# Kernel tuning notes

Hardware: AMD Instinct MI355X
Metric: run time of the kernel (lower is better)

The kernel has to match this reference:

```python
import jax, jax.numpy as jnp
import numpy as np


def setup_inputs() -> dict:
    key = jax.random.key(0)
    x = jax.random.normal(key, (4096, 512), dtype=jnp.float32)
    return {"x": x}


def reference(x):
    # Pairwise Euclidean distances for all (i, j) with i > j, flattened in the
    # same order as the original nested loop: (1,0),(2,0),(2,1),(3,0),...
    n = x.shape[0]
    sq = jnp.sum(x * x, axis=1)                      # [N]
    gram = x @ x.T                                   # [N, N]
    d2 = sq[:, None] + sq[None, :] - 2.0 * gram      # [N, N] squared dists
    ii, jj = jnp.tril_indices(n, k=-1)               # row-major lower triangle
    return jnp.sqrt(jnp.maximum(d2[ii, jj], 0.0))    # [N*(N-1)/2]
```

## Files before the change

kernel.cpp:

```cpp
#include <hip/hip_runtime.h>
#include <stdint.h>

#define N 4096
#define D 512
#define TILE 128
#define BK 128
#define KITERS (D / BK)
#define NB (N / TILE)
#define NOFF (NB * (NB - 1) / 2)
#define NBLK (NB * (NB + 1) / 2)

typedef float f32x4 __attribute__((ext_vector_type(4)));
typedef int   i32x8 __attribute__((ext_vector_type(8)));
typedef int   i32x4 __attribute__((ext_vector_type(4)));

__global__ __launch_bounds__(256) void prep_kernel(const float* __restrict__ x,
                                                   unsigned char* __restrict__ xq,
                                                   float* __restrict__ sq) {
    int row  = blockIdx.x * 4 + (threadIdx.x >> 6);
    int lane = threadIdx.x & 63;
    const float* xr = x + (size_t)row * D + lane * 8;
    float4 v0 = *reinterpret_cast<const float4*>(xr);
    float4 v1 = *reinterpret_cast<const float4*>(xr + 4);

    int w0 = __builtin_amdgcn_cvt_pk_fp8_f32(v0.x, v0.y, 0, false);
    w0     = __builtin_amdgcn_cvt_pk_fp8_f32(v0.z, v0.w, w0, true);
    int w1 = __builtin_amdgcn_cvt_pk_fp8_f32(v1.x, v1.y, 0, false);
    w1     = __builtin_amdgcn_cvt_pk_fp8_f32(v1.z, v1.w, w1, true);
    reinterpret_cast<int2*>(xq + (size_t)row * D)[lane] = make_int2(w0, w1);

    float s = v0.x * v0.x + v0.y * v0.y + v0.z * v0.z + v0.w * v0.w +
              v1.x * v1.x + v1.y * v1.y + v1.z * v1.z + v1.w * v1.w;
    #pragma unroll
    for (int off = 32; off > 0; off >>= 1) s += __shfl_down(s, off);
    if (lane == 0) sq[row] = s;
}

__global__ __launch_bounds__(512, 4) void pairdist_kernel(const unsigned char* __restrict__ xq,
                                                          const float* __restrict__ sq,
                                                          float* __restrict__ out) {
    __shared__ __align__(16) unsigned char As[TILE * BK];
    __shared__ __align__(16) unsigned char Bs[TILE * BK];

    int t = blockIdx.x;
    int bi, bj;
    if (t >= NOFF) {
        bi = bj = t - NOFF;
    } else {
        bi = (int)((sqrtf(8.0f * (float)t + 1.0f) + 1.0f) * 0.5f);
        while (bi * (bi - 1) / 2 > t) bi--;
        while ((bi + 1) * bi / 2 <= t) bi++;
        bj = t - bi * (bi - 1) / 2;
    }

    int tid  = threadIdx.x;
    int w    = tid >> 6;
    int lane = tid & 63;
    int quad = lane >> 4;
    int lr   = lane & 15;
    int wm   = w >> 1;
    int wn   = w & 1;

    const bool active = (bi != bj) || (wn == 0) || (wm >= 2);

    int srow   = lane >> 3;
    int schunk = lane & 7;
    int sw     = ((schunk ^ srow) << 4);
    const unsigned char* ga = xq + (size_t)(bi * TILE + w * 16 + srow) * D + sw;
    const unsigned char* gb = xq + (size_t)(bj * TILE + w * 16 + srow) * D + sw;
    unsigned char* la = As + w * 16 * BK;
    unsigned char* lb = Bs + w * 16 * BK;

    f32x4 acc[2][4];
    #pragma unroll
    for (int mt = 0; mt < 2; mt++)
        #pragma unroll
        for (int nt = 0; nt < 4; nt++)
            acc[mt][nt] = (f32x4)0.0f;

    for (int k0 = 0; k0 < D; k0 += BK) {
        __syncthreads();
        #pragma unroll
        for (int g = 0; g < 2; g++) {
            __builtin_amdgcn_global_load_lds(
                (const __attribute__((address_space(1))) void*)(ga + k0 + (size_t)g * 8 * D),
                (__attribute__((address_space(3))) void*)(la + g * 8 * BK), 16, 0, 0);
            __builtin_amdgcn_global_load_lds(
                (const __attribute__((address_space(1))) void*)(gb + k0 + (size_t)g * 8 * D),
                (__attribute__((address_space(3))) void*)(lb + g * 8 * BK), 16, 0, 0);
        }
        __syncthreads();

        if (active) {
            int c0 = (((2 * quad) ^ (lr & 7)) << 4);
            int c1 = c0 ^ 16;

            i32x8 af[2], bfr[4];
            #pragma unroll
            for (int mt = 0; mt < 2; mt++) {
                const unsigned char* rb = As + (wm * 32 + mt * 16 + lr) * BK;
                i32x4 lo = *reinterpret_cast<const i32x4*>(rb + c0);
                i32x4 hi = *reinterpret_cast<const i32x4*>(rb + c1);
                af[mt][0] = lo[0]; af[mt][1] = lo[1]; af[mt][2] = lo[2]; af[mt][3] = lo[3];
                af[mt][4] = hi[0]; af[mt][5] = hi[1]; af[mt][6] = hi[2]; af[mt][7] = hi[3];
            }
            #pragma unroll
            for (int nt = 0; nt < 4; nt++) {
                const unsigned char* rb = Bs + (wn * 64 + nt * 16 + lr) * BK;
                i32x4 lo = *reinterpret_cast<const i32x4*>(rb + c0);
                i32x4 hi = *reinterpret_cast<const i32x4*>(rb + c1);
                bfr[nt][0] = lo[0]; bfr[nt][1] = lo[1]; bfr[nt][2] = lo[2]; bfr[nt][3] = lo[3];
                bfr[nt][4] = hi[0]; bfr[nt][5] = hi[1]; bfr[nt][6] = hi[2]; bfr[nt][7] = hi[3];
            }

            #pragma unroll
            for (int mt = 0; mt < 2; mt++)
                #pragma unroll
                for (int nt = 0; nt < 4; nt++)
                    acc[mt][nt] = __builtin_amdgcn_mfma_scale_f32_16x16x128_f8f6f4(
                        af[mt], bfr[nt], acc[mt][nt],
                        0, 0,
                        0, 0x7F7F7F7F,
                        0, 0x7F7F7F7F);
        }
    }

    int ibase = bi * TILE + wm * 32;
    int jbase = bj * TILE + wn * 64;

    float sqi[2][4], sqj[4];
    #pragma unroll
    for (int mt = 0; mt < 2; mt++)
        #pragma unroll
        for (int tt = 0; tt < 4; tt++)
            sqi[mt][tt] = sq[ibase + mt * 16 + quad * 4 + tt];
    #pragma unroll
    for (int nt = 0; nt < 4; nt++)
        sqj[nt] = sq[jbase + nt * 16 + lr];

    if (bi != bj) {
        #pragma unroll
        for (int mt = 0; mt < 2; mt++) {
            #pragma unroll
            for (int tt = 0; tt < 4; tt++) {
                int i = ibase + mt * 16 + quad * 4 + tt;
                unsigned rowoff = (unsigned)(i * (i - 1) / 2);
                #pragma unroll
                for (int nt = 0; nt < 4; nt++) {
                    int j = jbase + nt * 16 + lr;
                    float d2 = sqi[mt][tt] + sqj[nt] - 2.0f * acc[mt][nt][tt];
                    out[rowoff + (unsigned)j] = __builtin_amdgcn_sqrtf(fmaxf(d2, 0.0f));
                }
            }
        }
    } else if (active) {
        #pragma unroll
        for (int mt = 0; mt < 2; mt++) {
            #pragma unroll
            for (int tt = 0; tt < 4; tt++) {
                int i = ibase + mt * 16 + quad * 4 + tt;
                unsigned rowoff = (unsigned)(i * (i - 1) / 2);
                #pragma unroll
                for (int nt = 0; nt < 4; nt++) {
                    int j = jbase + nt * 16 + lr;
                    if (j < i) {
                        float d2 = sqi[mt][tt] + sqj[nt] - 2.0f * acc[mt][nt][tt];
                        out[rowoff + (unsigned)j] = __builtin_amdgcn_sqrtf(fmaxf(d2, 0.0f));
                    }
                }
            }
        }
    }
}

extern "C" void kernel_launch(void* const* d_in, const int* in_sizes, int n_in,
                              void* d_out, int out_size, void* d_ws, size_t ws_size,
                              hipStream_t stream) {
    const float* x = (const float*)d_in[0];
    float* out = (float*)d_out;

    unsigned char* xq = (unsigned char*)d_ws;
    float* sq = (float*)((char*)d_ws + (size_t)N * D);

    prep_kernel<<<N / 4, 256, 0, stream>>>(x, xq, sq);

    pairdist_kernel<<<NBLK, 512, 0, stream>>>(xq, sq, out);
}
```

Baseline: 82.39 us.

## Switch to 64x128 rectangular tiles with 256-thread blocks for finer triangle coverage

Replaces the 128x128 square-tile triangular decomposition with 64-row by 128-column tiles processed by 4 waves per block, plus a new block-index-to-tile mapping that separates full tiles from diagonal partial tiles. The finer granularity wastes less work on the diagonal and yields more blocks for load balancing. In exchange each block reuses less data and issues more global-to-LDS traffic per output, and waves that are fully above the diagonal now exit early.

```diff
diff --git a/kernel.cpp b/kernel.cpp
--- a/kernel.cpp
+++ b/kernel.cpp
@@ -3,12 +3,14 @@
 
 #define N 4096
 #define D 512
-#define TILE 128
 #define BK 128
 #define KITERS (D / BK)
-#define NB (N / TILE)
-#define NOFF (NB * (NB - 1) / 2)
-#define NBLK (NB * (NB + 1) / 2)
+#define RG 64
+#define CP 128
+#define NRG (N / RG)
+#define NFULL 992
+#define NPART 64
+#define NBLK (NFULL + NPART)
 
 typedef float f32x4 __attribute__((ext_vector_type(4)));
 typedef int   i32x8 __attribute__((ext_vector_type(8)));
@@ -36,21 +38,24 @@
     if (lane == 0) sq[row] = s;
 }
 
-__global__ __launch_bounds__(512, 4) void pairdist_kernel(const unsigned char* __restrict__ xq,
+__global__ __launch_bounds__(256, 4) void pairdist_kernel(const unsigned char* __restrict__ xq,
                                                           const float* __restrict__ sq,
                                                           float* __restrict__ out) {
-    __shared__ __align__(16) unsigned char As[TILE * BK];
-    __shared__ __align__(16) unsigned char Bs[TILE * BK];
+    __shared__ __align__(16) unsigned char As[RG * BK];
+    __shared__ __align__(16) unsigned char Bs[CP * BK];
 
     int t = blockIdx.x;
-    int bi, bj;
-    if (t >= NOFF) {
-        bi = bj = t - NOFF;
+    int ri, cj;
+    if (t >= NFULL) {
+        int p = t - NFULL;
+        ri = p;
+        cj = p >> 1;
     } else {
-        bi = (int)((sqrtf(8.0f * (float)t + 1.0f) + 1.0f) * 0.5f);
-        while (bi * (bi - 1) / 2 > t) bi--;
-        while ((bi + 1) * bi / 2 <= t) bi++;
-        bj = t - bi * (bi - 1) / 2;
+        int a = (int)((sqrtf(4.0f * (float)t + 1.0f) + 1.0f) * 0.5f);
+        while (a * (a - 1) > t) a--;
+        while (a * (a + 1) <= t) a++;
+        if (t < a * a) { ri = 2 * a;     cj = t - a * (a - 1); }
+        else           { ri = 2 * a + 1; cj = t - a * a; }
     }
 
     int tid  = threadIdx.x;
@@ -61,15 +66,17 @@
     int wm   = w >> 1;
     int wn   = w & 1;
 
-    const bool active = (bi != bj) || (wn == 0) || (wm >= 2);
+    int ibase = ri * RG + wm * 32;
+    int jbase = cj * CP + wn * 64;
+    const bool active = (jbase <= ibase + 31);
 
     int srow   = lane >> 3;
     int schunk = lane & 7;
     int sw     = ((schunk ^ srow) << 4);
-    const unsigned char* ga = xq + (size_t)(bi * TILE + w * 16 + srow) * D + sw;
-    const unsigned char* gb = xq + (size_t)(bj * TILE + w * 16 + srow) * D + sw;
+    const unsigned char* ga = xq + (size_t)(ri * RG + w * 16 + srow) * D + sw;
+    const unsigned char* gb = xq + (size_t)(cj * CP + w * 32 + srow) * D + sw;
     unsigned char* la = As + w * 16 * BK;
-    unsigned char* lb = Bs + w * 16 * BK;
+    unsigned char* lb = Bs + w * 32 * BK;
 
     f32x4 acc[2][4];
     #pragma unroll
@@ -81,14 +88,15 @@
     for (int k0 = 0; k0 < D; k0 += BK) {
         __syncthreads();
         #pragma unroll
-        for (int g = 0; g < 2; g++) {
+        for (int g = 0; g < 2; g++)
             __builtin_amdgcn_global_load_lds(
                 (const __attribute__((address_space(1))) void*)(ga + k0 + (size_t)g * 8 * D),
                 (__attribute__((address_space(3))) void*)(la + g * 8 * BK), 16, 0, 0);
+        #pragma unroll
+        for (int g = 0; g < 4; g++)
             __builtin_amdgcn_global_load_lds(
                 (const __attribute__((address_space(1))) void*)(gb + k0 + (size_t)g * 8 * D),
                 (__attribute__((address_space(3))) void*)(lb + g * 8 * BK), 16, 0, 0);
-        }
         __syncthreads();
 
         if (active) {
@@ -125,8 +133,7 @@
         }
     }
 
-    int ibase = bi * TILE + wm * 32;
-    int jbase = bj * TILE + wn * 64;
+    if (!active) return;
 
     float sqi[2][4], sqj[4];
     #pragma unroll
@@ -138,7 +145,7 @@
     for (int nt = 0; nt < 4; nt++)
         sqj[nt] = sq[jbase + nt * 16 + lr];
 
-    if (bi != bj) {
+    if (jbase + 63 < ibase) {
         #pragma unroll
         for (int mt = 0; mt < 2; mt++) {
             #pragma unroll
@@ -153,7 +160,7 @@
                 }
             }
         }
-    } else if (active) {
+    } else {
         #pragma unroll
         for (int mt = 0; mt < 2; mt++) {
             #pragma unroll
@@ -184,5 +191,5 @@
 
     prep_kernel<<<N / 4, 256, 0, stream>>>(x, xq, sq);
 
-    pairdist_kernel<<<NBLK, 512, 0, stream>>>(xq, sq, out);
+    pairdist_kernel<<<NBLK, 256, 0, stream>>>(xq, sq, out);
 }
```

After: 81.28 us. About the same (-1.4%).

## Load MFMA fragments directly from global memory, dropping LDS staging and barriers

Applied to the files above, without the earlier changes.

Removes the shared-memory tiles and the per-iteration __syncthreads; each wave now reads its fp8 A/B fragments straight from global memory into registers, relying on L1/L2 for reuse across waves. Inactive waves on diagonal tiles return early, and fully-below-diagonal waves on diagonal tiles skip the per-element mask. This removes barrier and LDS traffic but raises redundant global/L2 reads, since tiles are no longer shared between the waves that use the same rows.

```diff
diff --git a/kernel.cpp b/kernel.cpp
--- a/kernel.cpp
+++ b/kernel.cpp
@@ -39,9 +39,6 @@
 __global__ __launch_bounds__(512, 4) void pairdist_kernel(const unsigned char* __restrict__ xq,
                                                           const float* __restrict__ sq,
                                                           float* __restrict__ out) {
-    __shared__ __align__(16) unsigned char As[TILE * BK];
-    __shared__ __align__(16) unsigned char Bs[TILE * BK];
-
     int t = blockIdx.x;
     int bi, bj;
     if (t >= NOFF) {
@@ -61,15 +58,11 @@
     int wm   = w >> 1;
     int wn   = w & 1;
 
+    int ibase = bi * TILE + wm * 32;
+    int jbase = bj * TILE + wn * 64;
+
     const bool active = (bi != bj) || (wn == 0) || (wm >= 2);
-
-    int srow   = lane >> 3;
-    int schunk = lane & 7;
-    int sw     = ((schunk ^ srow) << 4);
-    const unsigned char* ga = xq + (size_t)(bi * TILE + w * 16 + srow) * D + sw;
-    const unsigned char* gb = xq + (size_t)(bj * TILE + w * 16 + srow) * D + sw;
-    unsigned char* la = As + w * 16 * BK;
-    unsigned char* lb = Bs + w * 16 * BK;
+    const bool fullwave = (bi != bj) || (jbase + 63 < ibase);
 
     f32x4 acc[2][4];
     #pragma unroll
@@ -78,37 +71,27 @@
         for (int nt = 0; nt < 4; nt++)
             acc[mt][nt] = (f32x4)0.0f;
 
-    for (int k0 = 0; k0 < D; k0 += BK) {
-        __syncthreads();
+    if (active) {
+        const unsigned char* arow = xq + (size_t)(ibase + lr) * D + quad * 32;
+        const unsigned char* brow = xq + (size_t)(jbase + lr) * D + quad * 32;
+
         #pragma unroll
-        for (int g = 0; g < 2; g++) {
-            __builtin_amdgcn_global_load_lds(
-                (const __attribute__((address_space(1))) void*)(ga + k0 + (size_t)g * 8 * D),
-                (__attribute__((address_space(3))) void*)(la + g * 8 * BK), 16, 0, 0);
-            __builtin_amdgcn_global_load_lds(
-                (const __attribute__((address_space(1))) void*)(gb + k0 + (size_t)g * 8 * D),
-                (__attribute__((address_space(3))) void*)(lb + g * 8 * BK), 16, 0, 0);
-        }
-        __syncthreads();
-
-        if (active) {
-            int c0 = (((2 * quad) ^ (lr & 7)) << 4);
-            int c1 = c0 ^ 16;
-
+        for (int it = 0; it < KITERS; it++) {
+            const int k0 = it * BK;
             i32x8 af[2], bfr[4];
             #pragma unroll
             for (int mt = 0; mt < 2; mt++) {
-                const unsigned char* rb = As + (wm * 32 + mt * 16 + lr) * BK;
-                i32x4 lo = *reinterpret_cast<const i32x4*>(rb + c0);
-                i32x4 hi = *reinterpret_cast<const i32x4*>(rb + c1);
+                const unsigned char* p = arow + (size_t)(mt * 16) * D + k0;
+                i32x4 lo = *reinterpret_cast<const i32x4*>(p);
+                i32x4 hi = *reinterpret_cast<const i32x4*>(p + 16);
                 af[mt][0] = lo[0]; af[mt][1] = lo[1]; af[mt][2] = lo[2]; af[mt][3] = lo[3];
                 af[mt][4] = hi[0]; af[mt][5] = hi[1]; af[mt][6] = hi[2]; af[mt][7] = hi[3];
             }
             #pragma unroll
             for (int nt = 0; nt < 4; nt++) {
-                const unsigned char* rb = Bs + (wn * 64 + nt * 16 + lr) * BK;
-                i32x4 lo = *reinterpret_cast<const i32x4*>(rb + c0);
-                i32x4 hi = *reinterpret_cast<const i32x4*>(rb + c1);
+                const unsigned char* p = brow + (size_t)(nt * 16) * D + k0;
+                i32x4 lo = *reinterpret_cast<const i32x4*>(p);
+                i32x4 hi = *reinterpret_cast<const i32x4*>(p + 16);
                 bfr[nt][0] = lo[0]; bfr[nt][1] = lo[1]; bfr[nt][2] = lo[2]; bfr[nt][3] = lo[3];
                 bfr[nt][4] = hi[0]; bfr[nt][5] = hi[1]; bfr[nt][6] = hi[2]; bfr[nt][7] = hi[3];
             }
@@ -125,8 +108,7 @@
         }
     }
 
-    int ibase = bi * TILE + wm * 32;
-    int jbase = bj * TILE + wn * 64;
+    if (!active) return;
 
     float sqi[2][4], sqj[4];
     #pragma unroll
@@ -138,7 +120,7 @@
     for (int nt = 0; nt < 4; nt++)
         sqj[nt] = sq[jbase + nt * 16 + lr];
 
-    if (bi != bj) {
+    if (fullwave) {
         #pragma unroll
         for (int mt = 0; mt < 2; mt++) {
             #pragma unroll
@@ -153,7 +135,7 @@
                 }
             }
         }
-    } else if (active) {
+    } else {
         #pragma unroll
         for (int mt = 0; mt < 2; mt++) {
             #pragma unroll
```

Result: slower. 99.57 us (+20.8%).

## Give each wavefront an independent 32x64 triangular tile with private LDS

Applied to the files above, without the earlier changes.

Replaces the 128x128 block tiling, in which 8 waves share LDS tiles and synchronize with __syncthreads, with a per-wave decomposition. Each wavefront independently owns a 32x64 output tile, enumerated over the lower triangle so that diagonal blocks no longer carry idle waves. Each wave stages its own A/B slices through its own LDS region using global_load_lds and explicit waitcnt, and prefetches the next K slice while issuing MFMAs. This removes block-wide barriers and the wasted diagonal work, but loses operand sharing between waves, so global/L2 traffic increases and the hand-written waitcnt encodings carry correctness risk.

```diff
diff --git a/kernel.cpp b/kernel.cpp
--- a/kernel.cpp
+++ b/kernel.cpp
@@ -3,12 +3,13 @@
 
 #define N 4096
 #define D 512
-#define TILE 128
 #define BK 128
 #define KITERS (D / BK)
-#define NB (N / TILE)
-#define NOFF (NB * (NB - 1) / 2)
-#define NBLK (NB * (NB + 1) / 2)
+#define WTM 32
+#define WTN 64
+#define NGI (N / WTM)
+#define NTW 4160
+#define GRID (NTW / 4)
 
 typedef float f32x4 __attribute__((ext_vector_type(4)));
 typedef int   i32x8 __attribute__((ext_vector_type(8)));
@@ -36,40 +37,41 @@
     if (lane == 0) sq[row] = s;
 }
 
-__global__ __launch_bounds__(512, 4) void pairdist_kernel(const unsigned char* __restrict__ xq,
+__global__ __launch_bounds__(256, 3) void pairdist_kernel(const unsigned char* __restrict__ xq,
                                                           const float* __restrict__ sq,
                                                           float* __restrict__ out) {
-    __shared__ __align__(16) unsigned char As[TILE * BK];
-    __shared__ __align__(16) unsigned char Bs[TILE * BK];
-
-    int t = blockIdx.x;
-    int bi, bj;
-    if (t >= NOFF) {
-        bi = bj = t - NOFF;
-    } else {
-        bi = (int)((sqrtf(8.0f * (float)t + 1.0f) + 1.0f) * 0.5f);
-        while (bi * (bi - 1) / 2 > t) bi--;
-        while ((bi + 1) * bi / 2 <= t) bi++;
-        bj = t - bi * (bi - 1) / 2;
-    }
+    __shared__ __align__(16) unsigned char lds[4][12 * 1024];
 
     int tid  = threadIdx.x;
     int w    = tid >> 6;
     int lane = tid & 63;
     int quad = lane >> 4;
     int lr   = lane & 15;
-    int wm   = w >> 1;
-    int wn   = w & 1;
-
-    const bool active = (bi != bj) || (wn == 0) || (wm >= 2);
+
+    int t = blockIdx.x * 4 + w;
+
+    int a = (int)((sqrtf(4.0f * (float)t + 1.0f) - 1.0f) * 0.5f);
+    while (a * (a + 1) > t) a--;
+    while ((a + 1) * (a + 2) <= t) a++;
+    int gi, jg;
+    int r0 = t - a * (a + 1);
+    if (r0 <= a) { gi = 2 * a;     jg = r0; }
+    else         { gi = 2 * a + 1; jg = t - (a + 1) * (a + 1); }
+    const bool partial = (jg == (gi >> 1));
+
+    int ibase = gi * WTM;
+    int jbase = jg * WTN;
 
     int srow   = lane >> 3;
     int schunk = lane & 7;
     int sw     = ((schunk ^ srow) << 4);
-    const unsigned char* ga = xq + (size_t)(bi * TILE + w * 16 + srow) * D + sw;
-    const unsigned char* gb = xq + (size_t)(bj * TILE + w * 16 + srow) * D + sw;
-    unsigned char* la = As + w * 16 * BK;
-    unsigned char* lb = Bs + w * 16 * BK;
+    const unsigned char* ga = xq + (size_t)(ibase + srow) * D + sw;
+    const unsigned char* gb = xq + (size_t)(jbase + srow) * D + sw;
+    unsigned char* la = &lds[w][0];
+    unsigned char* lb = &lds[w][4 * 1024];
+
+    const int c0 = (((2 * quad) ^ (lr & 7)) << 4);
+    const int c1 = c0 ^ 16;
 
     f32x4 acc[2][4];
     #pragma unroll
@@ -78,55 +80,16 @@
         for (int nt = 0; nt < 4; nt++)
             acc[mt][nt] = (f32x4)0.0f;
 
-    for (int k0 = 0; k0 < D; k0 += BK) {
-        __syncthreads();
-        #pragma unroll
-        for (int g = 0; g < 2; g++) {
-            __builtin_amdgcn_global_load_lds(
-                (const __attribute__((address_space(1))) void*)(ga + k0 + (size_t)g * 8 * D),
-                (__attribute__((address_space(3))) void*)(la + g * 8 * BK), 16, 0, 0);
-            __builtin_amdgcn_global_load_lds(
-                (const __attribute__((address_space(1))) void*)(gb + k0 + (size_t)g * 8 * D),
-                (__attribute__((address_space(3))) void*)(lb + g * 8 * BK), 16, 0, 0);
-        }
-        __syncthreads();
-
-        if (active) {
-            int c0 = (((2 * quad) ^ (lr & 7)) << 4);
-            int c1 = c0 ^ 16;
-
-            i32x8 af[2], bfr[4];
-            #pragma unroll
-            for (int mt = 0; mt < 2; mt++) {
-                const unsigned char* rb = As + (wm * 32 + mt * 16 + lr) * BK;
-                i32x4 lo = *reinterpret_cast<const i32x4*>(rb + c0);
-                i32x4 hi = *reinterpret_cast<const i32x4*>(rb + c1);
-                af[mt][0] = lo[0]; af[mt][1] = lo[1]; af[mt][2] = lo[2]; af[mt][3] = lo[3];
-                af[mt][4] = hi[0]; af[mt][5] = hi[1]; af[mt][6] = hi[2]; af[mt][7] = hi[3];
-            }
-            #pragma unroll
-            for (int nt = 0; nt < 4; nt++) {
-                const unsigned char* rb = Bs + (wn * 64 + nt * 16 + lr) * BK;
-                i32x4 lo = *reinterpret_cast<const i32x4*>(rb + c0);
-                i32x4 hi = *reinterpret_cast<const i32x4*>(rb + c1);
-                bfr[nt][0] = lo[0]; bfr[nt][1] = lo[1]; bfr[nt][2] = lo[2]; bfr[nt][3] = lo[3];
-                bfr[nt][4] = hi[0]; bfr[nt][5] = hi[1]; bfr[nt][6] = hi[2]; bfr[nt][7] = hi[3];
-            }
-
-            #pragma unroll
-            for (int mt = 0; mt < 2; mt++)
-                #pragma unroll
-                for (int nt = 0; nt < 4; nt++)
-                    acc[mt][nt] = __builtin_amdgcn_mfma_scale_f32_16x16x128_f8f6f4(
-                        af[mt], bfr[nt], acc[mt][nt],
-                        0, 0,
-                        0, 0x7F7F7F7F,
-                        0, 0x7F7F7F7F);
-        }
-    }
-
-    int ibase = bi * TILE + wm * 32;
-    int jbase = bj * TILE + wn * 64;
+    #pragma unroll
+    for (int g = 0; g < 4; g++)
+        __builtin_amdgcn_global_load_lds(
+            (const __attribute__((address_space(1))) void*)(ga + (size_t)g * 8 * D),
+            (__attribute__((address_space(3))) void*)(la + g * 8 * BK), 16, 0, 0);
+    #pragma unroll
+    for (int g = 0; g < 8; g++)
+        __builtin_amdgcn_global_load_lds(
+            (const __attribute__((address_space(1))) void*)(gb + (size_t)g * 8 * D),
+            (__attribute__((address_space(3))) void*)(lb + g * 8 * BK), 16, 0, 0);
 
     float sqi[2][4], sqj[4];
     #pragma unroll
@@ -138,7 +101,57 @@
     for (int nt = 0; nt < 4; nt++)
         sqj[nt] = sq[jbase + nt * 16 + lr];
 
-    if (bi != bj) {
+    #pragma unroll
+    for (int it = 0; it < KITERS; it++) {
+        __builtin_amdgcn_s_waitcnt(0x0F70);
+        __builtin_amdgcn_sched_barrier(0);
+
+        i32x8 af[2], bfr[4];
+        #pragma unroll
+        for (int mt = 0; mt < 2; mt++) {
+            const unsigned char* rb = la + (mt * 16 + lr) * BK;
+            i32x4 lo = *reinterpret_cast<const i32x4*>(rb + c0);
+            i32x4 hi = *reinterpret_cast<const i32x4*>(rb + c1);
+            af[mt][0] = lo[0]; af[mt][1] = lo[1]; af[mt][2] = lo[2]; af[mt][3] = lo[3];
+            af[mt][4] = hi[0]; af[mt][5] = hi[1]; af[mt][6] = hi[2]; af[mt][7] = hi[3];
+        }
+        #pragma unroll
+        for (int nt = 0; nt < 4; nt++) {
+            const unsigned char* rb = lb + (nt * 16 + lr) * BK;
+            i32x4 lo = *reinterpret_cast<const i32x4*>(rb + c0);
+            i32x4 hi = *reinterpret_cast<const i32x4*>(rb + c1);
+            bfr[nt][0] = lo[0]; bfr[nt][1] = lo[1]; bfr[nt][2] = lo[2]; bfr[nt][3] = lo[3];
+            bfr[nt][4] = hi[0]; bfr[nt][5] = hi[1]; bfr[nt][6] = hi[2]; bfr[nt][7] = hi[3];
+        }
+
+        if (it + 1 < KITERS) {
+            __builtin_amdgcn_s_waitcnt(0xC07F);
+            __builtin_amdgcn_sched_barrier(0);
+            const int k0 = (it + 1) * BK;
+            #pragma unroll
+            for (int g = 0; g < 4; g++)
+                __builtin_amdgcn_global_load_lds(
+                    (const __attribute__((address_space(1))) void*)(ga + k0 + (size_t)g * 8 * D),
+                    (__attribute__((address_space(3))) void*)(la + g * 8 * BK), 16, 0, 0);
+            #pragma unroll
+            for (int g = 0; g < 8; g++)
+                __builtin_amdgcn_global_load_lds(
+                    (const __attribute__((address_space(1))) void*)(gb + k0 + (size_t)g * 8 * D),
+                    (__attribute__((address_space(3))) void*)(lb + g * 8 * BK), 16, 0, 0);
+        }
+
+        #pragma unroll
+        for (int mt = 0; mt < 2; mt++)
+            #pragma unroll
+            for (int nt = 0; nt < 4; nt++)
+                acc[mt][nt] = __builtin_amdgcn_mfma_scale_f32_16x16x128_f8f6f4(
+                    af[mt], bfr[nt], acc[mt][nt],
+                    0, 0,
+                    0, 0x7F7F7F7F,
+                    0, 0x7F7F7F7F);
+    }
+
+    if (!partial) {
         #pragma unroll
         for (int mt = 0; mt < 2; mt++) {
             #pragma unroll
@@ -153,7 +166,7 @@
                 }
             }
         }
-    } else if (active) {
+    } else {
         #pragma unroll
         for (int mt = 0; mt < 2; mt++) {
             #pragma unroll
@@ -184,5 +197,5 @@
 
     prep_kernel<<<N / 4, 256, 0, stream>>>(x, xq, sq);
 
-    pairdist_kernel<<<NBLK, 512, 0, stream>>>(xq, sq, out);
+    pairdist_kernel<<<GRID, 256, 0, stream>>>(xq, sq, out);
 }
```

Result: faster. 80.59 us (-2.2%).
